# Kernel tuning notes

Measured on AMD Instinct MI355X. Metric: run time of the kernel, lower is better.

## Reference

```python
import jax, jax.numpy as jnp
import numpy as np


def gcn_layer(x, W, b, src, dst):
    """GCNConv: out = D^{-1/2} (A + I) D^{-1/2} (x W) + b, aggregation at dst."""
    n = x.shape[0]
    h = x @ W  # [N, F_out]
    loops = jnp.arange(n, dtype=src.dtype)
    src_l = jnp.concatenate([src, loops])  # add self-loops
    dst_l = jnp.concatenate([dst, loops])
    ones = jnp.ones(dst_l.shape[0], dtype=x.dtype)
    deg = jax.ops.segment_sum(ones, dst_l, num_segments=n)  # in-degree incl. self-loop
    dinv = jnp.where(deg > 0, jax.lax.rsqrt(deg), 0.0)
    norm = dinv[src_l] * dinv[dst_l]  # [E+N]
    msg = h[src_l] * norm[:, None]  # gather + scale
    agg = jax.ops.segment_sum(msg, dst_l, num_segments=n)  # scatter-add
    return agg + b


def setup_inputs() -> dict:
    key = jax.random.key(0)
    k1, k2, k3, k4 = jax.random.split(key, 4)
    N, E = 1_000_000, 8_000_000
    x = jax.random.normal(k1, (N, 4), dtype=jnp.float32)
    edge_index = jax.random.randint(k2, (2, E), 0, N, dtype=jnp.int64)
    # glorot-ish init for the two GCN linear weights
    W1 = jax.random.normal(k3, (4, 64), dtype=jnp.float32) * (1.0 / np.sqrt(4))
    b1 = jnp.zeros((64,), dtype=jnp.float32)
    W2 = jax.random.normal(k4, (64, 2), dtype=jnp.float32) * (1.0 / np.sqrt(64))
    b2 = jnp.zeros((2,), dtype=jnp.float32)
    return {"x": x, "edge_index": edge_index, "W1": W1, "b1": b1, "W2": W2, "b2": b2}


def reference(x, edge_index, W1, b1, W2, b2):
    src, dst = edge_index[0], edge_index[1]
    h = jax.nn.relu(gcn_layer(x, W1, b1, src, dst))
    return gcn_layer(h, W2, b2, src, dst)
```

## Files before the change

### kernel.cpp

```cpp
#include <hip/hip_runtime.h>
#include <hip/hip_fp16.h>

#define CF_T 512
#define EPT 31
#define CHUNK (CF_T * EPT)
#define BB 11
#define BSZ (1 << BB)
#define BMASK (BSZ - 1)
#define SLICES 4
#define SSHIFT 18
#define MAXNKEY 2048
#define S2T 512
#define SCAP 4608
#define CP(i) ((i) + ((i) >> 5))

__device__ __forceinline__ int detect64(const int* __restrict__ ei) {
    return (ei[1] | ei[3] | ei[5] | ei[7] | ei[9] | ei[11] | ei[13] | ei[15]) == 0;
}
__device__ __forceinline__ int load_src(const int* __restrict__ ei, int e, int is64) {
    return is64 ? ei[2 * (size_t)e] : ei[(size_t)e];
}
__device__ __forceinline__ int load_dst(const int* __restrict__ ei, int E, int e, int is64) {
    return is64 ? ei[2 * ((size_t)E + e)] : ei[(size_t)E + e];
}
__device__ __forceinline__ unsigned int h2u(__half2 h) {
    union { __half2 h; unsigned int u; } c; c.h = h; return c.u;
}
__device__ __forceinline__ __half2 u2h(unsigned int u) {
    union { __half2 h; unsigned int u; } c; c.u = u; return c.h;
}

__global__ __launch_bounds__(256) void init_cur(
    unsigned int* __restrict__ gcur, int NKEY, unsigned int capk) {
    int k = blockIdx.x * 256 + threadIdx.x;
    if (k < NKEY) gcur[k] = (unsigned int)k * capk;
}

__global__ __launch_bounds__(CF_T) void chunk_sort_flush(
    const int* __restrict__ ei, int E, int NKEY,
    unsigned int* __restrict__ gcur, unsigned int* __restrict__ ebin,
    unsigned int total_cap) {
    __shared__ unsigned int cnt[MAXNKEY];
    __shared__ unsigned int gdst[MAXNKEY];
    __shared__ unsigned int ssum[CF_T];
    __shared__ unsigned int stg[CHUNK];
    int t = threadIdx.x, blk = blockIdx.x;
    for (int u = t; u < MAXNKEY; u += CF_T) cnt[u] = 0;
    __syncthreads();
    int is64 = detect64(ei);
    int lo = blk * CHUNK;
    int hi = lo + CHUNK; if (hi > E) hi = E;
    unsigned int rec[EPT];
    unsigned int ky[(EPT + 1) / 2];
#pragma unroll
    for (int j = 0; j < (EPT + 1) / 2; ++j) ky[j] = 0;
#pragma unroll
    for (int j = 0; j < EPT; ++j) {
        int e = lo + t + j * CF_T;
        if (e < hi) {
            int s = load_src(ei, e, is64);
            int d = load_dst(ei, E, e, is64);
            unsigned int key = ((unsigned int)(d >> BB) << 2) | (unsigned int)(s >> SSHIFT);
            rec[j] = ((unsigned int)s << BB) | (unsigned int)(d & BMASK);
            ky[j >> 1] |= key << ((j & 1) * 16);
            atomicAdd(&cnt[key], 1u);
        }
    }
    __syncthreads();
    unsigned int v[4];
    unsigned int sum = 0;
#pragma unroll
    for (int j = 0; j < 4; ++j) { unsigned int c = cnt[4 * t + j]; v[j] = sum; sum += c; }
    ssum[t] = sum;
    __syncthreads();
    for (int o = 1; o < CF_T; o <<= 1) {
        unsigned int x2 = (t >= o) ? ssum[t - o] : 0;
        __syncthreads();
        ssum[t] += x2;
        __syncthreads();
    }
    unsigned int base = t ? ssum[t - 1] : 0;
#pragma unroll
    for (int j = 0; j < 4; ++j) cnt[4 * t + j] = base + v[j];
    __syncthreads();
#pragma unroll
    for (int j = 0; j < EPT; ++j) {
        int e = lo + t + j * CF_T;
        if (e < hi) {
            unsigned int key = (ky[j >> 1] >> ((j & 1) * 16)) & 0xFFFFu;
            unsigned int pos = atomicAdd(&cnt[key], 1u);
            stg[pos] = rec[j];
        }
    }
    __syncthreads();
    for (int u = t; u < NKEY; u += CF_T) {
        unsigned int lst = u ? cnt[u - 1] : 0;
        unsigned int L = cnt[u] - lst;
        if (L) gdst[u] = atomicAdd(&gcur[u], L) - lst;
    }
    __syncthreads();
    int w = t >> 6, lane = t & 63, nw = CF_T >> 6;
    int g16 = lane >> 4, l16 = lane & 15;
    for (int u0 = w * 4; u0 < NKEY; u0 += nw * 4) {
        int u = u0 + g16;
        if (u < NKEY) {
            unsigned int lst = u ? cnt[u - 1] : 0;
            unsigned int en = cnt[u];
            for (unsigned int j = lst + l16; j < en; j += 16) {
                unsigned int gpos = gdst[u] + j;
                if (gpos < total_cap) ebin[gpos] = stg[j];
            }
        }
    }
}

__global__ __launch_bounds__(S2T) void sort2(
    const unsigned int* __restrict__ ebin, const unsigned int* __restrict__ gcur,
    unsigned int* __restrict__ ebin2, unsigned short* __restrict__ rp16,
    unsigned int capk) {
    __shared__ unsigned int cnt[CP(BSZ)];
    __shared__ unsigned int ssum[S2T];
    __shared__ unsigned int stg2[SCAP];
    int k = blockIdx.x, t = threadIdx.x;
    for (int j = t; j < CP(BSZ); j += S2T) cnt[j] = 0;
    __syncthreads();
    unsigned int kb = (unsigned int)k * capk;
    unsigned int ne_raw = gcur[k] - kb;
    int ne = (int)(ne_raw < capk ? ne_raw : capk);
    for (int i = t; i < ne; i += S2T) {
        unsigned int k11 = ebin[kb + i] & BMASK;
        atomicAdd(&cnt[CP(k11)], 1u);
    }
    __syncthreads();
    unsigned int loc[4];
    unsigned int s = 0;
#pragma unroll
    for (int j = 0; j < 4; ++j) { loc[j] = s; s += cnt[CP(4 * t + j)]; }
    ssum[t] = s;
    __syncthreads();
    for (int o = 1; o < S2T; o <<= 1) {
        unsigned int v = (t >= o) ? ssum[t - o] : 0;
        __syncthreads();
        ssum[t] += v;
        __syncthreads();
    }
    unsigned int tb = t ? ssum[t - 1] : 0;
    size_t rb = (size_t)k * BSZ;
#pragma unroll
    for (int j = 0; j < 4; ++j)
        rp16[rb + 4 * t + j] = (unsigned short)(tb + loc[j]);
#pragma unroll
    for (int j = 0; j < 4; ++j) cnt[CP(4 * t + j)] = tb + loc[j];
    __syncthreads();
    for (int i = t; i < ne; i += S2T) {
        unsigned int rec = ebin[kb + i];
        unsigned int pos = atomicAdd(&cnt[CP(rec & BMASK)], 1u);
        unsigned int v = rec >> BB;
        if (pos < SCAP) stg2[pos] = v;
        else ebin2[kb + pos] = v;
    }
    __syncthreads();
    int m = ne < SCAP ? ne : SCAP;
    for (int j = t; j < m; j += S2T) ebin2[kb + j] = stg2[j];
}

__global__ __launch_bounds__(256) void deg_prep(
    const unsigned short* __restrict__ rp16, const unsigned int* __restrict__ gcur,
    const float4* __restrict__ x, float* __restrict__ dinv, uint2* __restrict__ xs,
    int N, unsigned int capk) {
    int g = blockIdx.x * 256 + threadIdx.x;
    if (g >= N) return;
    int b = g >> BB, j = g & BMASK;
    unsigned int deg = 0;
#pragma unroll
    for (int s = 0; s < SLICES; ++s) {
        int key = (b << 2) | s;
        size_t rb = (size_t)key * BSZ;
        unsigned int st = rp16[rb + j];
        unsigned int en;
        if (j == BMASK) {
            unsigned int ner = gcur[key] - (unsigned int)key * capk;
            en = ner < capk ? ner : capk;
        } else en = rp16[rb + j + 1];
        deg += en - st;
    }
    float di = rsqrtf((float)(deg + 1u));
    dinv[g] = di;
    float4 v = x[g];
    uint2 p;
    p.x = h2u(__halves2half2(__float2half_rn(v.x * di), __float2half_rn(v.y * di)));
    p.y = h2u(__halves2half2(__float2half_rn(v.z * di), __float2half_rn(v.w * di)));
    xs[g] = p;
}

__global__ __launch_bounds__(256) void l1_gather(
    const unsigned int* __restrict__ ebin2, const unsigned short* __restrict__ rp16,
    const unsigned int* __restrict__ gcur, const uint2* __restrict__ xs,
    float4* __restrict__ partial, unsigned int capk) {
    int bid = blockIdx.x, t = threadIdx.x;
    int r = bid & 7, s = r & 3, half = r >> 2, q = bid >> 3;
    int b = q >> 2, sub = (half << 2) | (q & 3);
    int key = (b << 2) | s;
    int idx = (key << BB) + (sub << 8) + t;
    unsigned int kb = (unsigned int)key * capk;
    unsigned int st = kb + rp16[idx];
    unsigned int en;
    if ((sub == 7) && (t == 255)) {
        unsigned int ner = gcur[key] - kb;
        en = kb + (ner < capk ? ner : capk);
    } else en = kb + rp16[idx + 1];
    float ax = 0.0f, ay = 0.0f, az = 0.0f, aw = 0.0f;
    unsigned int e = st;
    for (; e + 2 <= en; e += 2) {
        unsigned int s0 = ebin2[e], s1 = ebin2[e + 1];
        uint2 r0 = xs[s0], r1 = xs[s1];
        __half2 a01 = u2h(r0.x), a23 = u2h(r0.y);
        __half2 b01 = u2h(r1.x), b23 = u2h(r1.y);
        ax += __half2float(__low2half(a01)) + __half2float(__low2half(b01));
        ay += __half2float(__high2half(a01)) + __half2float(__high2half(b01));
        az += __half2float(__low2half(a23)) + __half2float(__low2half(b23));
        aw += __half2float(__high2half(a23)) + __half2float(__high2half(b23));
    }
    if (e < en) {
        uint2 rr = xs[ebin2[e]];
        __half2 a01 = u2h(rr.x), a23 = u2h(rr.y);
        ax += __half2float(__low2half(a01));
        ay += __half2float(__high2half(a01));
        az += __half2float(__low2half(a23));
        aw += __half2float(__high2half(a23));
    }
    partial[idx] = make_float4(ax, ay, az, aw);
}

__global__ __launch_bounds__(256) void l1_reduce_mlp(
    const float4* __restrict__ partial, const uint2* __restrict__ xs,
    const float* __restrict__ dinv,
    const float* __restrict__ W1, const float* __restrict__ b1,
    const float* __restrict__ W2, unsigned int* __restrict__ ps, int N) {
    __shared__ float sW1[256];
    __shared__ float sb1[64];
    __shared__ float sW2[128];
    int t = threadIdx.x;
    sW1[t] = W1[t];
    if (t < 64) sb1[t] = b1[t];
    if (t < 128) sW2[t] = W2[t];
    __syncthreads();
    int i = blockIdx.x * 256 + t;
    if (i >= N) return;
    int bucket = i >> BB, j = i & BMASK;
    float axs = 0.0f, ays = 0.0f, azs = 0.0f, aws = 0.0f;
    size_t kb = (size_t)bucket * SLICES;
    for (int s = 0; s < SLICES; ++s) {
        float4 v = partial[(kb + s) * BSZ + j];
        axs += v.x; ays += v.y; azs += v.z; aws += v.w;
    }
    float di = dinv[i];
    uint2 raw = xs[i];
    __half2 h01 = u2h(raw.x), h23 = u2h(raw.y);
    float ax = (axs + __half2float(__low2half(h01))) * di;
    float ay = (ays + __half2float(__high2half(h01))) * di;
    float az = (azs + __half2float(__low2half(h23))) * di;
    float aw = (aws + __half2float(__high2half(h23))) * di;
    float p0 = 0.0f, p1 = 0.0f;
#pragma unroll
    for (int k = 0; k < 64; ++k) {
        float h = fmaf(ax, sW1[k],
                  fmaf(ay, sW1[64 + k],
                  fmaf(az, sW1[128 + k],
                  fmaf(aw, sW1[192 + k], sb1[k]))));
        h = fmaxf(h, 0.0f);
        p0 = fmaf(h, sW2[2 * k + 0], p0);
        p1 = fmaf(h, sW2[2 * k + 1], p1);
    }
    ps[i] = h2u(__halves2half2(__float2half_rn(p0 * di), __float2half_rn(p1 * di)));
}

__global__ __launch_bounds__(256) void l2_gather(
    const unsigned int* __restrict__ ebin2, const unsigned short* __restrict__ rp16,
    const unsigned int* __restrict__ gcur, const unsigned int* __restrict__ ps,
    float2* __restrict__ partial, unsigned int capk) {
    int bid = blockIdx.x, t = threadIdx.x;
    int r = bid & 7, s = r & 3, half = r >> 2, q = bid >> 3;
    int b = q >> 2, sub = (half << 2) | (q & 3);
    int key = (b << 2) | s;
    int idx = (key << BB) + (sub << 8) + t;
    unsigned int kb = (unsigned int)key * capk;
    unsigned int st = kb + rp16[idx];
    unsigned int en;
    if ((sub == 7) && (t == 255)) {
        unsigned int ner = gcur[key] - kb;
        en = kb + (ner < capk ? ner : capk);
    } else en = kb + rp16[idx + 1];
    float s0 = 0.0f, s1 = 0.0f;
    unsigned int e = st;
    for (; e + 2 <= en; e += 2) {
        unsigned int a = ebin2[e], bb = ebin2[e + 1];
        unsigned int ra = ps[a], rb2 = ps[bb];
        __half2 ha = u2h(ra), hb = u2h(rb2);
        s0 += __half2float(__low2half(ha)) + __half2float(__low2half(hb));
        s1 += __half2float(__high2half(ha)) + __half2float(__high2half(hb));
    }
    if (e < en) {
        __half2 h = u2h(ps[ebin2[e]]);
        s0 += __half2float(__low2half(h));
        s1 += __half2float(__high2half(h));
    }
    partial[idx] = make_float2(s0, s1);
}

__global__ __launch_bounds__(256) void l2_reduce(
    const float2* __restrict__ partial, const unsigned int* __restrict__ ps,
    const float* __restrict__ dinv, const float* __restrict__ b2,
    float2* __restrict__ out, int N) {
    int i = blockIdx.x * 256 + threadIdx.x;
    if (i >= N) return;
    int bucket = i >> BB, j = i & BMASK;
    float s0 = 0.0f, s1 = 0.0f;
    size_t kb = (size_t)bucket * SLICES;
    for (int s = 0; s < SLICES; ++s) {
        float2 v = partial[(kb + s) * BSZ + j];
        s0 += v.x; s1 += v.y;
    }
    float di = dinv[i];
    __half2 h = u2h(ps[i]);
    float2 rr;
    rr.x = fmaf(s0 + __half2float(__low2half(h)), di, b2[0]);
    rr.y = fmaf(s1 + __half2float(__high2half(h)), di, b2[1]);
    out[i] = rr;
}

static inline size_t align256(size_t v) { return (v + 255) & ~(size_t)255; }

extern "C" void kernel_launch(void* const* d_in, const int* in_sizes, int n_in,
                              void* d_out, int out_size, void* d_ws, size_t ws_size,
                              hipStream_t stream) {
    const float* x  = (const float*)d_in[0];
    const int*   ei = (const int*)d_in[1];
    const float* W1 = (const float*)d_in[2];
    const float* b1 = (const float*)d_in[3];
    const float* W2 = (const float*)d_in[4];
    const float* b2 = (const float*)d_in[5];

    const int N = in_sizes[0] / 4;
    const int E = in_sizes[1] / 2;
    const int NB = (N + BSZ - 1) >> BB;
    const int NKEY = NB * SLICES;
    const int NBLKc = (E + CHUNK - 1) / CHUNK;

    unsigned int capk = (unsigned int)((E + NKEY - 1) / NKEY);
    capk = capk + capk / 8 + 128;
    capk = (capk + 63u) & ~63u;
    const unsigned int total_cap = (unsigned int)NKEY * capk;

    size_t o = 0;
    size_t o_cur  = o; o = align256(o + (size_t)NKEY * 4);
    size_t o_dinv = o; o = align256(o + (size_t)N * 4);
    size_t o_xs   = o; o = align256(o + (size_t)N * 8);
    size_t o_ps   = o; o = align256(o + (size_t)N * 4);
    size_t o_eb2  = o; o = align256(o + (size_t)total_cap * 4);
    size_t o_rp   = o; o = align256(o + (size_t)NKEY * BSZ * 2);
    size_t o_R    = o;
    size_t o_ebin = o_R;

    char* ws = (char*)d_ws;
    unsigned int*   gcur  = (unsigned int*)(ws + o_cur);
    float*          dinv  = (float*)(ws + o_dinv);
    uint2*          xs    = (uint2*)(ws + o_xs);
    unsigned int*   ps    = (unsigned int*)(ws + o_ps);
    unsigned int*   ebin2 = (unsigned int*)(ws + o_eb2);
    unsigned short* rp16  = (unsigned short*)(ws + o_rp);
    unsigned int*   ebin  = (unsigned int*)(ws + o_ebin);
    float4*         part4 = (float4*)(ws + o_R);
    float2*         part2 = (float2*)(ws + o_R);

    init_cur<<<(NKEY + 255) / 256, 256, 0, stream>>>(gcur, NKEY, capk);
    chunk_sort_flush<<<NBLKc, CF_T, 0, stream>>>(ei, E, NKEY, gcur, ebin, total_cap);
    sort2<<<NKEY, S2T, 0, stream>>>(ebin, gcur, ebin2, rp16, capk);
    deg_prep<<<(N + 255) / 256, 256, 0, stream>>>(rp16, gcur, (const float4*)x,
                                                  dinv, xs, N, capk);
    l1_gather<<<NB * 32, 256, 0, stream>>>(ebin2, rp16, gcur, xs, part4, capk);
    l1_reduce_mlp<<<(N + 255) / 256, 256, 0, stream>>>(part4, xs, dinv, W1, b1, W2, ps, N);
    l2_gather<<<NB * 32, 256, 0, stream>>>(ebin2, rp16, gcur, ps, part2, capk);
    l2_reduce<<<(N + 255) / 256, 256, 0, stream>>>(part2, ps, dinv, b2, (float2*)d_out, N);
}
```

Baseline: 298.5 us.

## Fuse per-slice gathers with reductions into single per-node kernels

```diff
diff --git a/kernel.cpp b/kernel.cpp
--- a/kernel.cpp
+++ b/kernel.cpp
@@ -193,69 +193,60 @@
     xs[g] = p;
 }
 
-__global__ __launch_bounds__(256) void l1_gather(
+__global__ __launch_bounds__(256) void l1_fused(
     const unsigned int* __restrict__ ebin2, const unsigned short* __restrict__ rp16,
     const unsigned int* __restrict__ gcur, const uint2* __restrict__ xs,
-    float4* __restrict__ partial, unsigned int capk) {
-    int bid = blockIdx.x, t = threadIdx.x;
-    int r = bid & 7, s = r & 3, half = r >> 2, q = bid >> 3;
-    int b = q >> 2, sub = (half << 2) | (q & 3);
-    int key = (b << 2) | s;
-    int idx = (key << BB) + (sub << 8) + t;
-    unsigned int kb = (unsigned int)key * capk;
-    unsigned int st = kb + rp16[idx];
-    unsigned int en;
-    if ((sub == 7) && (t == 255)) {
-        unsigned int ner = gcur[key] - kb;
-        en = kb + (ner < capk ? ner : capk);
-    } else en = kb + rp16[idx + 1];
-    float ax = 0.0f, ay = 0.0f, az = 0.0f, aw = 0.0f;
-    unsigned int e = st;
-    for (; e + 2 <= en; e += 2) {
-        unsigned int s0 = ebin2[e], s1 = ebin2[e + 1];
-        uint2 r0 = xs[s0], r1 = xs[s1];
-        __half2 a01 = u2h(r0.x), a23 = u2h(r0.y);
-        __half2 b01 = u2h(r1.x), b23 = u2h(r1.y);
-        ax += __half2float(__low2half(a01)) + __half2float(__low2half(b01));
-        ay += __half2float(__high2half(a01)) + __half2float(__high2half(b01));
-        az += __half2float(__low2half(a23)) + __half2float(__low2half(b23));
-        aw += __half2float(__high2half(a23)) + __half2float(__high2half(b23));
-    }
-    if (e < en) {
-        uint2 rr = xs[ebin2[e]];
-        __half2 a01 = u2h(rr.x), a23 = u2h(rr.y);
-        ax += __half2float(__low2half(a01));
-        ay += __half2float(__high2half(a01));
-        az += __half2float(__low2half(a23));
-        aw += __half2float(__high2half(a23));
-    }
-    partial[idx] = make_float4(ax, ay, az, aw);
-}
-
-__global__ __launch_bounds__(256) void l1_reduce_mlp(
-    const float4* __restrict__ partial, const uint2* __restrict__ xs,
     const float* __restrict__ dinv,
     const float* __restrict__ W1, const float* __restrict__ b1,
-    const float* __restrict__ W2, unsigned int* __restrict__ ps, int N) {
+    const float* __restrict__ W2, unsigned int* __restrict__ ps,
+    int N, unsigned int capk) {
     __shared__ float sW1[256];
     __shared__ float sb1[64];
     __shared__ float sW2[128];
-    int t = threadIdx.x;
+    int t = threadIdx.x, bid = blockIdx.x;
     sW1[t] = W1[t];
     if (t < 64) sb1[t] = b1[t];
     if (t < 128) sW2[t] = W2[t];
     __syncthreads();
-    int i = blockIdx.x * 256 + t;
-    if (i >= N) return;
-    int bucket = i >> BB, j = i & BMASK;
+    int g = bid * 256 + t;
+    if (g >= N) return;
+    int b = g >> BB, j = g & BMASK;
+    int xcd = bid & 7;
     float axs = 0.0f, ays = 0.0f, azs = 0.0f, aws = 0.0f;
-    size_t kb = (size_t)bucket * SLICES;
-    for (int s = 0; s < SLICES; ++s) {
-        float4 v = partial[(kb + s) * BSZ + j];
-        axs += v.x; ays += v.y; azs += v.z; aws += v.w;
-    }
-    float di = dinv[i];
-    uint2 raw = xs[i];
+#pragma unroll
+    for (int p = 0; p < SLICES; ++p) {
+        int s = (xcd + p) & 3;
+        int key = (b << 2) | s;
+        unsigned int kb = (unsigned int)key * capk;
+        size_t rb = (size_t)key * BSZ;
+        unsigned int st = kb + rp16[rb + j];
+        unsigned int en;
+        if (j == BMASK) {
+            unsigned int ner = gcur[key] - kb;
+            en = kb + (ner < capk ? ner : capk);
+        } else en = kb + rp16[rb + j + 1];
+        unsigned int e = st;
+        for (; e + 2 <= en; e += 2) {
+            unsigned int s0 = ebin2[e], s1 = ebin2[e + 1];
+            uint2 r0 = xs[s0], r1 = xs[s1];
+            __half2 a01 = u2h(r0.x), a23 = u2h(r0.y);
+            __half2 b01 = u2h(r1.x), b23 = u2h(r1.y);
+            axs += __half2float(__low2half(a01)) + __half2float(__low2half(b01));
+            ays += __half2float(__high2half(a01)) + __half2float(__high2half(b01));
+            azs += __half2float(__low2half(a23)) + __half2float(__low2half(b23));
+            aws += __half2float(__high2half(a23)) + __half2float(__high2half(b23));
+        }
+        if (e < en) {
+            uint2 rr = xs[ebin2[e]];
+            __half2 a01 = u2h(rr.x), a23 = u2h(rr.y);
+            axs += __half2float(__low2half(a01));
+            ays += __half2float(__high2half(a01));
+            azs += __half2float(__low2half(a23));
+            aws += __half2float(__high2half(a23));
+        }
+    }
+    float di = dinv[g];
+    uint2 raw = xs[g];
     __half2 h01 = u2h(raw.x), h23 = u2h(raw.y);
     float ax = (axs + __half2float(__low2half(h01))) * di;
     float ay = (ays + __half2float(__high2half(h01))) * di;
@@ -272,61 +263,52 @@
         p0 = fmaf(h, sW2[2 * k + 0], p0);
         p1 = fmaf(h, sW2[2 * k + 1], p1);
     }
-    ps[i] = h2u(__halves2half2(__float2half_rn(p0 * di), __float2half_rn(p1 * di)));
-}
-
-__global__ __launch_bounds__(256) void l2_gather(
+    ps[g] = h2u(__halves2half2(__float2half_rn(p0 * di), __float2half_rn(p1 * di)));
+}
+
+__global__ __launch_bounds__(256) void l2_fused(
     const unsigned int* __restrict__ ebin2, const unsigned short* __restrict__ rp16,
     const unsigned int* __restrict__ gcur, const unsigned int* __restrict__ ps,
-    float2* __restrict__ partial, unsigned int capk) {
-    int bid = blockIdx.x, t = threadIdx.x;
-    int r = bid & 7, s = r & 3, half = r >> 2, q = bid >> 3;
-    int b = q >> 2, sub = (half << 2) | (q & 3);
-    int key = (b << 2) | s;
-    int idx = (key << BB) + (sub << 8) + t;
-    unsigned int kb = (unsigned int)key * capk;
-    unsigned int st = kb + rp16[idx];
-    unsigned int en;
-    if ((sub == 7) && (t == 255)) {
-        unsigned int ner = gcur[key] - kb;
-        en = kb + (ner < capk ? ner : capk);
-    } else en = kb + rp16[idx + 1];
+    const float* __restrict__ dinv, const float* __restrict__ b2,
+    float2* __restrict__ out, int N, unsigned int capk) {
+    int t = threadIdx.x, bid = blockIdx.x;
+    int g = bid * 256 + t;
+    if (g >= N) return;
+    int b = g >> BB, j = g & BMASK;
+    int xcd = bid & 7;
     float s0 = 0.0f, s1 = 0.0f;
-    unsigned int e = st;
-    for (; e + 2 <= en; e += 2) {
-        unsigned int a = ebin2[e], bb = ebin2[e + 1];
-        unsigned int ra = ps[a], rb2 = ps[bb];
-        __half2 ha = u2h(ra), hb = u2h(rb2);
-        s0 += __half2float(__low2half(ha)) + __half2float(__low2half(hb));
-        s1 += __half2float(__high2half(ha)) + __half2float(__high2half(hb));
-    }
-    if (e < en) {
-        __half2 h = u2h(ps[ebin2[e]]);
-        s0 += __half2float(__low2half(h));
-        s1 += __half2float(__high2half(h));
-    }
-    partial[idx] = make_float2(s0, s1);
-}
-
-__global__ __launch_bounds__(256) void l2_reduce(
-    const float2* __restrict__ partial, const unsigned int* __restrict__ ps,
-    const float* __restrict__ dinv, const float* __restrict__ b2,
-    float2* __restrict__ out, int N) {
-    int i = blockIdx.x * 256 + threadIdx.x;
-    if (i >= N) return;
-    int bucket = i >> BB, j = i & BMASK;
-    float s0 = 0.0f, s1 = 0.0f;
-    size_t kb = (size_t)bucket * SLICES;
-    for (int s = 0; s < SLICES; ++s) {
-        float2 v = partial[(kb + s) * BSZ + j];
-        s0 += v.x; s1 += v.y;
-    }
-    float di = dinv[i];
-    __half2 h = u2h(ps[i]);
+#pragma unroll
+    for (int p = 0; p < SLICES; ++p) {
+        int s = (xcd + p) & 3;
+        int key = (b << 2) | s;
+        unsigned int kb = (unsigned int)key * capk;
+        size_t rb = (size_t)key * BSZ;
+        unsigned int st = kb + rp16[rb + j];
+        unsigned int en;
+        if (j == BMASK) {
+            unsigned int ner = gcur[key] - kb;
+            en = kb + (ner < capk ? ner : capk);
+        } else en = kb + rp16[rb + j + 1];
+        unsigned int e = st;
+        for (; e + 2 <= en; e += 2) {
+            unsigned int a = ebin2[e], bb = ebin2[e + 1];
+            unsigned int ra = ps[a], rb2 = ps[bb];
+            __half2 ha = u2h(ra), hb = u2h(rb2);
+            s0 += __half2float(__low2half(ha)) + __half2float(__low2half(hb));
+            s1 += __half2float(__high2half(ha)) + __half2float(__high2half(hb));
+        }
+        if (e < en) {
+            __half2 h = u2h(ps[ebin2[e]]);
+            s0 += __half2float(__low2half(h));
+            s1 += __half2float(__high2half(h));
+        }
+    }
+    float di = dinv[g];
+    __half2 h = u2h(ps[g]);
     float2 rr;
     rr.x = fmaf(s0 + __half2float(__low2half(h)), di, b2[0]);
     rr.y = fmaf(s1 + __half2float(__high2half(h)), di, b2[1]);
-    out[i] = rr;
+    out[g] = rr;
 }
 
 static inline size_t align256(size_t v) { return (v + 255) & ~(size_t)255; }
@@ -346,6 +328,7 @@
     const int NB = (N + BSZ - 1) >> BB;
     const int NKEY = NB * SLICES;
     const int NBLKc = (E + CHUNK - 1) / CHUNK;
+    const int NBLKn = (N + 255) / 256;
 
     unsigned int capk = (unsigned int)((E + NKEY - 1) / NKEY);
     capk = capk + capk / 8 + 128;
@@ -359,8 +342,7 @@
     size_t o_ps   = o; o = align256(o + (size_t)N * 4);
     size_t o_eb2  = o; o = align256(o + (size_t)total_cap * 4);
     size_t o_rp   = o; o = align256(o + (size_t)NKEY * BSZ * 2);
-    size_t o_R    = o;
-    size_t o_ebin = o_R;
+    size_t o_ebin = o; o = align256(o + (size_t)total_cap * 4);
 
     char* ws = (char*)d_ws;
     unsigned int*   gcur  = (unsigned int*)(ws + o_cur);
@@ -370,16 +352,11 @@
     unsigned int*   ebin2 = (unsigned int*)(ws + o_eb2);
     unsigned short* rp16  = (unsigned short*)(ws + o_rp);
     unsigned int*   ebin  = (unsigned int*)(ws + o_ebin);
-    float4*         part4 = (float4*)(ws + o_R);
-    float2*         part2 = (float2*)(ws + o_R);
 
     init_cur<<<(NKEY + 255) / 256, 256, 0, stream>>>(gcur, NKEY, capk);
     chunk_sort_flush<<<NBLKc, CF_T, 0, stream>>>(ei, E, NKEY, gcur, ebin, total_cap);
     sort2<<<NKEY, S2T, 0, stream>>>(ebin, gcur, ebin2, rp16, capk);
-    deg_prep<<<(N + 255) / 256, 256, 0, stream>>>(rp16, gcur, (const float4*)x,
-                                                  dinv, xs, N, capk);
-    l1_gather<<<NB * 32, 256, 0, stream>>>(ebin2, rp16, gcur, xs, part4, capk);
-    l1_reduce_mlp<<<(N + 255) / 256, 256, 0, stream>>>(part4, xs, dinv, W1, b1, W2, ps, N);
-    l2_gather<<<NB * 32, 256, 0, stream>>>(ebin2, rp16, gcur, ps, part2, capk);
-    l2_reduce<<<(N + 255) / 256, 256, 0, stream>>>(part2, ps, dinv, b2, (float2*)d_out, N);
-}
+    deg_prep<<<NBLKn, 256, 0, stream>>>(rp16, gcur, (const float4*)x, dinv, xs, N, capk);
+    l1_fused<<<NBLKn, 256, 0, stream>>>(ebin2, rp16, gcur, xs, dinv, W1, b1, W2, ps, N, capk);
+    l2_fused<<<NBLKn, 256, 0, stream>>>(ebin2, rp16, gcur, ps, dinv, b2, (float2*)d_out, N, capk);
+}
```

Measured after the change: 292.7 us. About the same (-2.0%).
